# Kernel tuning notes

Measured on AMD Instinct MI355X. Metric: run time of the kernel, lower is better.

The kernel has to match this reference:

```python
import jax, jax.numpy as jnp
import numpy as np
from jax import lax

DN = ('NCHW', 'OIHW', 'NCHW')

def conv(x, w, groups=1):
    return lax.conv_general_dilated(x, w, (1, 1), 'SAME',
                                    feature_group_count=groups,
                                    dimension_numbers=DN)

def layernorm_cf(x, w, b, eps=1e-6):
    # channels-first LayerNorm over dim=1
    u = x.mean(1, keepdims=True)
    s = ((x - u) ** 2).mean(1, keepdims=True)
    xn = (x - u) / jnp.sqrt(s + eps)
    return w[None, :, None, None] * xn + b[None, :, None, None]

def l2norm(x, eps=1e-12):
    n = jnp.sqrt(jnp.sum(x * x, axis=-1, keepdims=True))
    return x / jnp.maximum(n, eps)

def setup_inputs() -> dict:
    key = jax.random.key(0)
    ks = jax.random.split(key, 16)
    B, C, H, W = 4, 192, 128, 128
    heads = 6
    hidden = int(C * 2.66)  # 510
    s = 0.02
    rn = lambda k, shp: jax.random.normal(k, shp, dtype=jnp.float32) * s
    return {
        'x': jax.random.normal(ks[0], (B, C, H, W), dtype=jnp.float32),
        'ln_w': jnp.ones((C,), jnp.float32),
        'ln_b': jnp.zeros((C,), jnp.float32),
        'temperature': jnp.ones((heads, 1, 1), jnp.float32),
        'q_w': rn(ks[1], (C, C, 1, 1)),
        'q_dw_w': rn(ks[2], (C, 1, 3, 3)),
        'kv_w': rn(ks[3], (2 * C, C, 1, 1)),
        'kv_dw_w': rn(ks[4], (2 * C, 1, 3, 3)),
        'proj_w': rn(ks[5], (C, C, 1, 1)),
        'pos_embed': rn(ks[6], (1, C, 1, 1)),
        'pos_q_w': rn(ks[7], (C, C, 1, 1)),
        'pos_k_w': rn(ks[8], (C, C, 1, 1)),
        'sel_in_w': rn(ks[9], (hidden, C, 3, 3)),
        'sel_dw_w': rn(ks[10], (hidden, 1, 3, 3)),
        'sel_out_w': rn(ks[11], (C, hidden, 3, 3)),
        'alpha': jnp.float32(0.5),
    }

def reference(x, ln_w, ln_b, temperature, q_w, q_dw_w, kv_w, kv_dw_w,
              proj_w, pos_embed, pos_q_w, pos_k_w,
              sel_in_w, sel_dw_w, sel_out_w, alpha):
    b, c, h, w = x.shape
    heads = temperature.shape[0]
    ch = c // heads
    n = h * w

    # --- CFA on norm_x (norm_x == norm_y since both are norm(x)) ---
    norm_x = layernorm_cf(x, ln_w, ln_b)
    q = conv(conv(norm_x, q_w), q_dw_w, groups=c)
    kv = conv(conv(norm_x, kv_w), kv_dw_w, groups=2 * c)
    k, v = jnp.split(kv, 2, axis=1)

    q = q.reshape(b, heads, ch, n)
    k = k.reshape(b, heads, ch, n)
    v = v.reshape(b, heads, ch, n)

    qn = l2norm(q)
    kn = l2norm(k)
    attn = jax.nn.softmax(jnp.einsum('bhcn,bhdn->bhcd', qn, kn) * temperature[None], axis=-1)
    out = jnp.einsum('bhcd,bhdn->bhcn', attn, v)

    pos_x = norm_x + pos_embed
    pos_q = conv(pos_x, pos_q_w).reshape(b, heads, ch, n)
    pos_k = conv(pos_x, pos_k_w).reshape(b, heads, ch, n)
    pos_attn = jax.nn.softmax(jnp.einsum('bhcn,bhdn->bhcd', pos_q, pos_k), axis=-1)
    pos_out = jnp.einsum('bhcd,bhdn->bhcn', pos_attn, v)

    out = (out + pos_out).reshape(b, c, h, w)
    out = conv(out, proj_w)
    x = x + alpha * out

    # --- SEL (conv-FFN) ---
    nx = layernorm_cf(x, ln_w, ln_b)
    g = conv(nx, sel_in_w)
    g = conv(g, sel_dw_w, groups=g.shape[1])
    g = jax.nn.silu(g)
    g = conv(g, sel_out_w)
    x = x + (1.0 - alpha) * g
    return x
```

## Files before the change

### kernel.cpp

```cpp
#include <hip/hip_runtime.h>
#include <hip/hip_bf16.h>
#include <stdint.h>

#define DEVI __device__ __forceinline__

typedef __attribute__((ext_vector_type(8))) unsigned short us8;
typedef __attribute__((ext_vector_type(8))) __bf16 bf16x8;
typedef __attribute__((ext_vector_type(4))) float f32x4;

#define BB 4
#define CC 192
#define HH 128
#define NPIX 16384
#define MTOT 65536
#define HEADS 6

DEVI float b2f(unsigned short u){ return __uint_as_float(((unsigned)u)<<16); }
DEVI unsigned short f2b(float f){
  unsigned u = __float_as_uint(f);
  return (unsigned short)((u + 0x7fffu + ((u>>16)&1u)) >> 16);
}

DEVI void gload16(const void* g, void* l){
  __builtin_amdgcn_global_load_lds((const __attribute__((address_space(1))) unsigned int*)g,
                                   (__attribute__((address_space(3))) unsigned int*)l,
                                   16, 0, 0);
}

__global__ __launch_bounds__(256)
void ln1_k(const float* __restrict__ x, const float* __restrict__ lnw,
           const float* __restrict__ lnb, unsigned short* __restrict__ nx)
{
  __shared__ float tile[CC*65];
  __shared__ float stats[64*2];
  int gbase = blockIdx.x * 64;
  int b = gbase >> 14; int n0 = gbase & (NPIX-1);
  for (int idx = threadIdx.x; idx < CC*64; idx += 256){
    int c = idx >> 6, j = idx & 63;
    tile[c*65 + j] = x[((size_t)b*CC + c)*NPIX + n0 + j];
  }
  __syncthreads();
  if (threadIdx.x < 64){
    int j = threadIdx.x;
    float s = 0.f, ss = 0.f;
    for (int c = 0; c < CC; c++){ float v = tile[c*65 + j]; s += v; ss += v*v; }
    float mu = s * (1.f/CC);
    float var = ss * (1.f/CC) - mu*mu;
    stats[j*2] = mu; stats[j*2+1] = rsqrtf(var + 1e-6f);
  }
  __syncthreads();
  for (int idx = threadIdx.x; idx < CC*64; idx += 256){
    int c = idx % CC, j = idx / CC;
    float v = (tile[c*65 + j] - stats[j*2]) * stats[j*2+1] * lnw[c] + lnb[c];
    nx[(size_t)(gbase + j)*CC + c] = f2b(v);
  }
}

__global__ __launch_bounds__(256)
void ln2_k(const float* __restrict__ x2, const float* __restrict__ lnw,
           const float* __restrict__ lnb, unsigned short* __restrict__ nx)
{
  int gm = blockIdx.x*4 + (threadIdx.x >> 6);
  int lane = threadIdx.x & 63;
  const float* row = x2 + (size_t)gm*CC;
  float v0 = row[lane], v1 = row[lane+64], v2 = row[lane+128];
  float s = v0+v1+v2, ss = v0*v0+v1*v1+v2*v2;
  #pragma unroll
  for (int o = 32; o >= 1; o >>= 1){
    s  += __shfl_xor(s,  o);
    ss += __shfl_xor(ss, o);
  }
  float mu = s * (1.f/CC);
  float rstd = rsqrtf(ss*(1.f/CC) - mu*mu + 1e-6f);
  unsigned short* o0 = nx + (size_t)gm*CC;
  o0[lane]     = f2b((v0-mu)*rstd*lnw[lane]     + lnb[lane]);
  o0[lane+64]  = f2b((v1-mu)*rstd*lnw[lane+64]  + lnb[lane+64]);
  o0[lane+128] = f2b((v2-mu)*rstd*lnw[lane+128] + lnb[lane+128]);
}

template<int EPI, int NSLICES>
__global__ __launch_bounds__(512, 2)
void gemm256_k(const unsigned short* __restrict__ A, int strideA,
               const unsigned short* __restrict__ W, int Ktot,
               int NcolsW, int NcolsStore, int outStride, int colBlocks,
               unsigned short* __restrict__ outB,
               const float* __restrict__ res, float* __restrict__ outF,
               const float* __restrict__ alphaP,
               const unsigned short* __restrict__ zerop)
{
  __shared__ unsigned short lds[65536];

  const int tid = threadIdx.x;
  const int l  = tid & 63;
  const int w  = tid >> 6;
  const int wm = w >> 2;
  const int wn = w & 3;

  const int q8 = gridDim.x >> 3;
  const int bid = (blockIdx.x & 7)*q8 + (blockIdx.x >> 3);
  const int mblk = bid / colBlocks;
  const int nblk = bid - mblk*colBlocks;
  const int m0 = mblk*256, co0 = nblk*256;

  int rowT[4], slotX[4];
  #pragma unroll
  for (int i = 0; i < 4; i++){
    rowT[i]  = (w*4 + i)*8 + (l >> 3);
    slotX[i] = (l & 7) ^ (rowT[i] & 7);
  }
  const unsigned short* baseA[4];
  int hhA[4], wwA[4];
  #pragma unroll
  for (int i = 0; i < 4; i++){
    int gm = m0 + rowT[i];
    int np = gm & (NPIX-1);
    hhA[i] = np >> 7; wwA[i] = np & 127;
    baseA[i] = A + (size_t)gm*strideA + (slotX[i] << 3);
  }
  const unsigned short* baseB[4];
  bool bval[4];
  #pragma unroll
  for (int i = 0; i < 4; i++){
    int co = co0 + rowT[i];
    bval[i] = (co < NcolsW);
    baseB[i] = bval[i] ? (W + (size_t)co*Ktot + (slotX[i] << 3)) : (zerop + (l << 3));
  }

  const int NT = Ktot >> 6;

  auto STAGE = [&](int ts){
    int buf = ts & 1;
    unsigned short* la = lds + buf*16384;
    unsigned short* lb = lds + 32768 + buf*16384;
    int ci0, dy = 0, dx = 0;
    if constexpr (NSLICES == 1){ ci0 = ts << 6; }
    else { int cib = ts/9, s = ts - cib*9; ci0 = cib << 6; dy = s/3 - 1; dx = s - (s/3)*3 - 1; }
    #pragma unroll
    for (int i = 0; i < 4; i++){
      const unsigned short* srcA;
      if constexpr (NSLICES == 1){
        srcA = baseA[i] + ci0;
      } else {
        int h2 = hhA[i] + dy, w2 = wwA[i] + dx;
        srcA = ((unsigned)h2 < 128u && (unsigned)w2 < 128u)
             ? (baseA[i] + (dy*HH + dx)*strideA + ci0)
             : (zerop + (l << 3));
      }
      gload16(srcA, la + (w*4 + i)*512);
    }
    #pragma unroll
    for (int i = 0; i < 4; i++){
      const unsigned short* srcB = bval[i] ? (baseB[i] + (ts << 6)) : baseB[i];
      gload16(srcB, lb + (w*4 + i)*512);
    }
  };

  f32x4 acc[8][4] = {};

  STAGE(0);
  asm volatile("s_waitcnt vmcnt(0)" ::: "memory");
  __syncthreads();

  for (int t = 0; t < NT; ++t){
    if (t + 1 < NT) STAGE(t + 1);
    const unsigned short* la = lds + (t & 1)*16384;
    const unsigned short* lb = lds + 32768 + (t & 1)*16384;
    __builtin_amdgcn_s_setprio(1);
    #pragma unroll
    for (int kk = 0; kk < 2; kk++){
      int ks = kk*4 + (l >> 4);
      bf16x8 bf[4];
      #pragma unroll
      for (int nf = 0; nf < 4; nf++){
        int rb = wn*64 + nf*16 + (l & 15);
        bf[nf] = *(const bf16x8*)(lb + rb*64 + ((ks ^ (rb & 7)) << 3));
      }
      #pragma unroll
      for (int mf = 0; mf < 8; mf++){
        int rm = wm*128 + mf*16 + (l & 15);
        bf16x8 af = *(const bf16x8*)(la + rm*64 + ((ks ^ (rm & 7)) << 3));
        #pragma unroll
        for (int nf = 0; nf < 4; nf++)
          acc[mf][nf] = __builtin_amdgcn_mfma_f32_16x16x32_bf16(af, bf[nf], acc[mf][nf], 0, 0, 0);
      }
    }
    __builtin_amdgcn_s_setprio(0);
    __syncthreads();
  }

  float alpha = (EPI == 2) ? (1.f - *alphaP) : 0.f;
  #pragma unroll
  for (int mf = 0; mf < 8; mf++){
    int r0 = m0 + wm*128 + mf*16 + ((l >> 4) << 2);
    #pragma unroll
    for (int nf = 0; nf < 4; nf++){
      int co = co0 + wn*64 + nf*16 + (l & 15);
      if (co < NcolsStore){
        #pragma unroll
        for (int r = 0; r < 4; r++){
          int gm = r0 + r;
          float v = acc[mf][nf][r];
          if constexpr (EPI == 0){
            outB[(size_t)gm*outStride + co] = f2b(v);
          } else {
            int b = gm >> 14, np = gm & (NPIX-1);
            outF[((size_t)b*CC + co)*NPIX + np] = res[(size_t)gm*CC + co] + alpha*v;
          }
        }
      }
    }
  }
}

template<int EPI, int NSLICES>
__global__ __launch_bounds__(256, 2)
void gemm_k(const unsigned short* __restrict__ A, int strideA,
            const unsigned short* __restrict__ W, int Ktot, int sliceC,
            int NcolsW, int NcolsStore, int outStride, int colBlocks,
            unsigned short* __restrict__ outB,
            const float* __restrict__ bias,
            const float* __restrict__ res,
            float* __restrict__ outF,
            const float* __restrict__ alphaP,
            const unsigned short* __restrict__ zerop)
{
  __shared__ unsigned short lds[2*128*64];
  unsigned short* ldsA = lds;
  unsigned short* ldsB = lds + 128*64;

  const int tid = threadIdx.x;
  const int lane = tid & 63;
  const int wv = tid >> 6;
  const int q8 = gridDim.x >> 3;
  const int bid = (blockIdx.x & 7)*q8 + (blockIdx.x >> 3);
  const int mblk = bid / colBlocks;
  const int nblk = bid - mblk*colBlocks;
  const int m0 = mblk*128, co0 = nblk*128;

  const int jT = lane & 7;
  int rowT[4];
  #pragma unroll
  for (int i = 0; i < 4; i++) rowT[i] = ((wv*4 + i)*64 + lane) >> 3;

  const unsigned short* bsrc[4];
  #pragma unroll
  for (int i = 0; i < 4; i++){
    int co = co0 + rowT[i];
    int jj = jT ^ (rowT[i] & 7);
    bsrc[i] = (co < NcolsW) ? (W + (size_t)co*Ktot + (jj << 3))
                            : (zerop + (lane << 3));
  }

  const unsigned short* asrc[4];
  int gmA[4], jjA[4];
  #pragma unroll
  for (int i = 0; i < 4; i++){
    gmA[i] = m0 + rowT[i];
    jjA[i] = jT ^ (rowT[i] & 7);
    asrc[i] = A + (size_t)gmA[i]*strideA + (jjA[i] << 3);
  }

  f32x4 acc[4][4] = {};
  int ci0 = 0, s = 0, dy = -1, dx = -1;

  for (int k0 = 0; k0 < Ktot; k0 += 64){
    if constexpr (NSLICES == 1){
      #pragma unroll
      for (int i = 0; i < 4; i++){
        gload16(asrc[i], (char*)ldsA + (wv*4 + i)*1024);
        asrc[i] += 64;
      }
    } else {
      #pragma unroll
      for (int i = 0; i < 4; i++){
        int gm = gmA[i];
        int np = gm & (NPIX-1);
        int hh = np >> 7, ww = np & 127;
        int h2 = hh + dy, w2 = ww + dx;
        const unsigned short* src = ((unsigned)h2 < 128u && (unsigned)w2 < 128u)
          ? (A + (size_t)(gm + dy*HH + dx)*strideA + ci0 + (jjA[i] << 3))
          : (zerop + (lane << 3));
        gload16(src, (char*)ldsA + (wv*4 + i)*1024);
      }
    }
    #pragma unroll
    for (int i = 0; i < 4; i++){
      gload16(bsrc[i], (char*)ldsB + (wv*4 + i)*1024);
      bsrc[i] += 64;
    }
    asm volatile("s_waitcnt vmcnt(0)" ::: "memory");
    __syncthreads();

    #pragma unroll
    for (int kk = 0; kk < 2; kk++){
      bf16x8 af[4], bfr[4];
      int kb = kk*64 + ((lane >> 4) << 4);
      #pragma unroll
      for (int mi = 0; mi < 4; mi++){
        int rm = (wv >> 1)*64 + mi*16 + (lane & 15);
        int off = rm*128 + (kb ^ ((rm & 7) << 4));
        af[mi] = *(const bf16x8*)((const char*)ldsA + off);
      }
      #pragma unroll
      for (int ni = 0; ni < 4; ni++){
        int rb = (wv & 1)*64 + ni*16 + (lane & 15);
        int off = rb*128 + (kb ^ ((rb & 7) << 4));
        bfr[ni] = *(const bf16x8*)((const char*)ldsB + off);
      }
      #pragma unroll
      for (int mi = 0; mi < 4; mi++)
        #pragma unroll
        for (int ni = 0; ni < 4; ni++)
          acc[mi][ni] = __builtin_amdgcn_mfma_f32_16x16x32_bf16(af[mi], bfr[ni], acc[mi][ni], 0, 0, 0);
    }
    __syncthreads();

    if constexpr (NSLICES > 1){
      s++; if (s == 9){ s = 0; ci0 += 64; }
      dy = s/3 - 1; dx = s - (s/3)*3 - 1;
    }
  }
  (void)sliceC;

  float alpha = 0.f;
  if (EPI == 1) alpha = *alphaP;
  if (EPI == 2) alpha = 1.f - *alphaP;
  const int colb = co0 + (wv & 1)*64;
  const int rowb = m0 + (wv >> 1)*64;
  #pragma unroll
  for (int mi = 0; mi < 4; mi++){
    int r0 = rowb + mi*16 + ((lane >> 4) << 2);
    #pragma unroll
    for (int ni = 0; ni < 4; ni++){
      int co = colb + ni*16 + (lane & 15);
      if (co < NcolsStore){
        float bv = (EPI == 0 && bias) ? bias[co] : 0.f;
        #pragma unroll
        for (int r = 0; r < 4; r++){
          int gm = r0 + r;
          float v = acc[mi][ni][r];
          if constexpr (EPI == 0){
            outB[(size_t)gm*outStride + co] = f2b(v + bv);
          } else if constexpr (EPI == 1){
            int b = gm >> 14, np = gm & (NPIX-1);
            outF[(size_t)gm*CC + co] = res[((size_t)b*CC + co)*NPIX + np] + alpha*v;
          } else {
            int b = gm >> 14, np = gm & (NPIX-1);
            outF[((size_t)b*CC + co)*NPIX + np] = res[(size_t)gm*CC + co] + alpha*v;
          }
        }
      }
    }
  }
}

template<int NCHV, int DOSILU>
__global__ __launch_bounds__(256)
void dw_k(const unsigned short* __restrict__ src, int strideS,
          const float* __restrict__ wtT, int wstride,
          unsigned short* __restrict__ dst, int strideD)
{
  const int q8 = gridDim.x >> 3;
  const int bid = (blockIdx.x & 7)*q8 + (blockIdx.x >> 3);
  int idx = bid*256 + threadIdx.x;
  int gm = idx / NCHV;
  int cb = idx - gm*NCHV;
  int c = cb*8;
  int np = gm & (NPIX-1);
  int hh = np >> 7, ww = np & 127;
  float acc[8] = {0,0,0,0,0,0,0,0};
  #pragma unroll
  for (int s = 0; s < 9; s++){
    int dy = s/3 - 1, dx = s%3 - 1;
    int h2 = hh + dy, w2 = ww + dx;
    if ((unsigned)h2 < 128u && (unsigned)w2 < 128u){
      us8 t = *(const us8*)(src + (size_t)(gm + dy*HH + dx)*strideS + c);
      f32x4 w0 = *(const f32x4*)(wtT + s*wstride + c);
      f32x4 w1 = *(const f32x4*)(wtT + s*wstride + c + 4);
      #pragma unroll
      for (int j = 0; j < 4; j++){
        acc[j]   += b2f(t[j])   * w0[j];
        acc[4+j] += b2f(t[4+j]) * w1[j];
      }
    }
  }
  us8 o;
  #pragma unroll
  for (int j = 0; j < 8; j++){
    float v = acc[j];
    if (DOSILU) v = v / (1.f + __expf(-v));
    o[j] = f2b(v);
  }
  *(us8*)(dst + (size_t)gm*strideD + c) = o;
}

__global__ __launch_bounds__(192)
void sumsq_k(const unsigned short* __restrict__ q, int stride, float* __restrict__ part)
{
  int b = blockIdx.x >> 5, ch = blockIdx.x & 31;
  int c = threadIdx.x;
  const unsigned short* base = q + ((size_t)b*NPIX + ch*512)*stride + c;
  float acc = 0.f;
  for (int r = 0; r < 512; r++){ float v = b2f(base[(size_t)r*stride]); acc += v*v; }
  part[(size_t)(b*32 + ch)*CC + c] = acc;
}

__global__ __launch_bounds__(256)
void pairdot_k(const unsigned short* __restrict__ qb, const unsigned short* __restrict__ kb,
               int stride, float* __restrict__ Spart)
{
  __shared__ float qs[32][129];
  __shared__ float ks[32][129];
  int bh = blockIdx.x >> 3;
  int chunk = blockIdx.x & 7;
  int b = bh / HEADS, h = bh - b*HEADS;
  int t = threadIdx.x;
  int cP = t >> 3;
  int dg = t & 7;
  size_t gm0 = (size_t)b*NPIX + chunk*2048;
  int r = t >> 1, hf = t & 1;
  float acc0=0, acc1=0, acc2=0, acc3=0;
  for (int sub = 0; sub < 16; sub++){
    __syncthreads();
    {
      const unsigned short* pq = qb + (gm0 + sub*128 + r)*stride + h*32 + hf*16;
      const unsigned short* pk = kb + (gm0 + sub*128 + r)*stride + h*32 + hf*16;
      us8 a0 = *(const us8*)pq; us8 a1 = *(const us8*)(pq + 8);
      us8 b0 = *(const us8*)pk; us8 b1 = *(const us8*)(pk + 8);
      #pragma unroll
      for (int j = 0; j < 8; j++){
        qs[hf*16 + j][r]     = b2f(a0[j]);
        qs[hf*16 + 8 + j][r] = b2f(a1[j]);
        ks[hf*16 + j][r]     = b2f(b0[j]);
        ks[hf*16 + 8 + j][r] = b2f(b1[j]);
      }
    }
    __syncthreads();
    for (int n = 0; n < 128; n++){
      float qv = qs[cP][n];
      acc0 += qv * ks[dg*4+0][n];
      acc1 += qv * ks[dg*4+1][n];
      acc2 += qv * ks[dg*4+2][n];
      acc3 += qv * ks[dg*4+3][n];
    }
  }
  float* o = Spart + (size_t)blockIdx.x*1024 + cP*32 + dg*4;
  o[0]=acc0; o[1]=acc1; o[2]=acc2; o[3]=acc3;
}

__global__ __launch_bounds__(64)
void smax_k(const float* __restrict__ Spos, const float* __restrict__ Scfa,
            const float* __restrict__ qnp, const float* __restrict__ knp,
            const float* __restrict__ temp, float* __restrict__ att)
{
  int bh = blockIdx.x; int b = bh / HEADS, h = bh - b*HEADS;
  __shared__ float kn[32];
  int t = threadIdx.x;
  if (t < 32){
    float ss = 0.f;
    for (int ck = 0; ck < 32; ck++) ss += knp[((size_t)b*32 + ck)*CC + h*32 + t];
    kn[t] = fmaxf(sqrtf(ss), 1e-12f);
  }
  __syncthreads();
  if (t >= 32) return;
  int c = t;
  float ssq = 0.f;
  for (int ck = 0; ck < 32; ck++) ssq += qnp[((size_t)b*32 + ck)*CC + h*32 + c];
  float qn = fmaxf(sqrtf(ssq), 1e-12f);
  float rowS[32], rowP[32];
  #pragma unroll
  for (int d = 0; d < 32; d++){
    float sv = 0.f, pv = 0.f;
    for (int ck = 0; ck < 8; ck++){
      sv += Scfa[(size_t)(bh*8 + ck)*1024 + c*32 + d];
      pv += Spos[(size_t)(bh*8 + ck)*1024 + c*32 + d];
    }
    rowS[d] = sv; rowP[d] = pv;
  }
  float tv = temp[h];
  float m1 = -3e38f, m2 = -3e38f;
  #pragma unroll
  for (int d = 0; d < 32; d++){
    rowS[d] = rowS[d] / (qn*kn[d]) * tv;
    m1 = fmaxf(m1, rowS[d]);
    m2 = fmaxf(m2, rowP[d]);
  }
  float s1 = 0.f, s2 = 0.f;
  #pragma unroll
  for (int d = 0; d < 32; d++){
    rowS[d] = __expf(rowS[d] - m1); s1 += rowS[d];
    rowP[d] = __expf(rowP[d] - m2); s2 += rowP[d];
  }
  float r1 = 1.f/s1, r2 = 1.f/s2;
  #pragma unroll
  for (int d = 0; d < 32; d++)
    att[(size_t)bh*1024 + c*32 + d] = rowS[d]*r1 + rowP[d]*r2;
}

__global__ __launch_bounds__(256)
void pv_k(const float* __restrict__ att, const unsigned short* __restrict__ vd, int stride,
          unsigned short* __restrict__ outT)
{
  __shared__ float As[32][33];
  int bh = blockIdx.x >> 8; int mc = blockIdx.x & 255;
  int b = bh / HEADS, h = bh - b*HEADS;
  int t = threadIdx.x;
  for (int i = t; i < 1024; i += 256) As[i >> 5][i & 31] = att[(size_t)bh*1024 + i];
  __syncthreads();
  int gm = b*NPIX + mc*64 + (t >> 2);
  int cq = t & 3;
  const unsigned short* vp = vd + (size_t)gm*stride + h*32;
  float acc[8] = {0,0,0,0,0,0,0,0};
  for (int d = 0; d < 32; d++){
    float vv = b2f(vp[d]);
    #pragma unroll
    for (int j = 0; j < 8; j++) acc[j] += As[cq*8 + j][d] * vv;
  }
  us8 o;
  #pragma unroll
  for (int j = 0; j < 8; j++) o[j] = f2b(acc[j]);
  *(us8*)(outT + (size_t)gm*CC + h*32 + cq*8) = o;
}

__global__ void castcopy_k(const float* __restrict__ s, unsigned short* __restrict__ d, int n){
  int i = blockIdx.x*256 + threadIdx.x; if (i < n) d[i] = f2b(s[i]);
}
__global__ void prepselin_k(const float* __restrict__ s, unsigned short* __restrict__ d){
  int i = blockIdx.x*256 + threadIdx.x;
  if (i >= 510*1728) return;
  int co = i / 1728, rem = i - co*1728;
  int chunk = rem >> 6, e = rem & 63;
  int cib = chunk / 9, sl = chunk - cib*9;
  int ci = cib*64 + e;
  d[i] = f2b(s[(size_t)(co*192 + ci)*9 + sl]);
}
__global__ void prepselout_k(const float* __restrict__ s, unsigned short* __restrict__ d){
  int i = blockIdx.x*256 + threadIdx.x;
  if (i >= 192*4608) return;
  int co = i / 4608, rem = i - co*4608;
  int chunk = rem >> 6, e = rem & 63;
  int cib = chunk / 9, sl = chunk - cib*9;
  int ci = cib*64 + e;
  d[i] = (ci < 510) ? f2b(s[(size_t)(co*510 + ci)*9 + sl]) : (unsigned short)0;
}
__global__ void prepbias_k(const float* __restrict__ pq, const float* __restrict__ pk,
                           const float* __restrict__ pe, float* __restrict__ bias){
  int r = blockIdx.x*64 + threadIdx.x;
  if (r >= 960) return;
  float s = 0.f;
  if (r < 384){
    const float* Wp = (r < 192) ? pq : pk;
    int co = (r < 192) ? r : r - 192;
    for (int ci = 0; ci < 192; ci++) s += Wp[co*192 + ci]*pe[ci];
  }
  bias[r] = s;
}
__global__ void prepdwT_k(const float* __restrict__ qdw, const float* __restrict__ kvdw,
                          const float* __restrict__ seldw,
                          float* __restrict__ wqkv, float* __restrict__ wsel){
  int i = blockIdx.x*256 + threadIdx.x;
  if (i < 9*576){
    int s = i / 576, c = i - s*576;
    wqkv[i] = (c < 192) ? qdw[c*9 + s] : kvdw[(size_t)(c-192)*9 + s];
  }
  int j = i - 9*576;
  if (j >= 0 && j < 9*512){
    int s = j / 512, c = j - s*512;
    wsel[j] = (c < 510) ? seldw[(size_t)c*9 + s] : 0.f;
  }
}

extern "C" void kernel_launch(void* const* d_in, const int* in_sizes, int n_in,
                              void* d_out, int out_size, void* d_ws, size_t ws_size,
                              hipStream_t stream)
{
  const float* x       = (const float*)d_in[0];
  const float* ln_w    = (const float*)d_in[1];
  const float* ln_b    = (const float*)d_in[2];
  const float* temp    = (const float*)d_in[3];
  const float* q_w     = (const float*)d_in[4];
  const float* q_dw    = (const float*)d_in[5];
  const float* kv_w    = (const float*)d_in[6];
  const float* kv_dw   = (const float*)d_in[7];
  const float* proj_w  = (const float*)d_in[8];
  const float* pos_e   = (const float*)d_in[9];
  const float* posq_w  = (const float*)d_in[10];
  const float* posk_w  = (const float*)d_in[11];
  const float* selin_w = (const float*)d_in[12];
  const float* seldw_w = (const float*)d_in[13];
  const float* selout_w= (const float*)d_in[14];
  const float* alphaP  = (const float*)d_in[15];

  char* ws = (char*)d_ws;
  unsigned short* zerop  = (unsigned short*)(ws + 0);
  float* biasC           = (float*)(ws + 4096);
  float* Spos            = (float*)(ws + 8192);
  float* Scfa            = (float*)(ws + 794624);
  float* qnp             = (float*)(ws + 1581056);
  float* knp             = (float*)(ws + 1679360);
  float* att             = (float*)(ws + 1777664);
  unsigned short* WC     = (unsigned short*)(ws + 2097152);
  unsigned short* Wproj  = (unsigned short*)(ws + 2465792);
  unsigned short* Wselin = (unsigned short*)(ws + 2539520);
  unsigned short* Wselout= (unsigned short*)(ws + 4302080);
  float* WdwQKV          = (float*)(ws + 6071552);
  float* WdwSEL          = (float*)(ws + 6092288);
  unsigned short* normx  = (unsigned short*)(ws + 8388608);
  unsigned short* outT   = normx;
  unsigned short* qp     = (unsigned short*)(ws + 33554432);
  float*          x2     = (float*)(ws + 33554432);
  unsigned short* nx     = (unsigned short*)(ws + 83886080);
  unsigned short* g2     = (unsigned short*)(ws + 83886080);
  unsigned short* qkvd   = (unsigned short*)(ws + 159383552);
  unsigned short* g      = qkvd;

  hipMemsetAsync(zerop, 0, 4096, stream);

  castcopy_k<<<144, 256, 0, stream>>>(posq_w, WC,          36864);
  castcopy_k<<<144, 256, 0, stream>>>(posk_w, WC + 36864,  36864);
  castcopy_k<<<144, 256, 0, stream>>>(q_w,    WC + 73728,  36864);
  castcopy_k<<<288, 256, 0, stream>>>(kv_w,   WC + 110592, 73728);
  castcopy_k<<<144, 256, 0, stream>>>(proj_w, Wproj,       36864);
  prepselin_k<<<3443, 256, 0, stream>>>(selin_w, Wselin);
  prepselout_k<<<3456, 256, 0, stream>>>(selout_w, Wselout);
  prepbias_k<<<15, 64, 0, stream>>>(posq_w, posk_w, pos_e, biasC);
  prepdwT_k<<<39, 256, 0, stream>>>(q_dw, kv_dw, seldw_w, WdwQKV, WdwSEL);

  ln1_k<<<1024, 256, 0, stream>>>(x, ln_w, ln_b, normx);
  gemm_k<0,1><<<512*8, 256, 0, stream>>>(normx, 192, WC, 192, 192, 960, 960, 960, 8,
                                         qp, biasC, nullptr, nullptr, nullptr, zerop);
  pairdot_k<<<192, 256, 0, stream>>>(qp, qp + 192, 960, Spos);
  dw_k<72,0><<<18432, 256, 0, stream>>>(qp + 384, 960, WdwQKV, 576, qkvd, 576);
  sumsq_k<<<128, 192, 0, stream>>>(qkvd,       576, qnp);
  sumsq_k<<<128, 192, 0, stream>>>(qkvd + 192, 576, knp);
  pairdot_k<<<192, 256, 0, stream>>>(qkvd, qkvd + 192, 576, Scfa);
  smax_k<<<24, 64, 0, stream>>>(Spos, Scfa, qnp, knp, temp, att);
  pv_k<<<24*256, 256, 0, stream>>>(att, qkvd + 384, 576, outT);
  gemm_k<1,1><<<512*2, 256, 0, stream>>>(outT, 192, Wproj, 192, 192, 192, 192, 0, 2,
                                         nullptr, nullptr, x, x2, alphaP, zerop);
  ln2_k<<<16384, 256, 0, stream>>>(x2, ln_w, ln_b, nx);
  gemm256_k<0,9><<<512, 512, 0, stream>>>(nx, 192, Wselin, 1728, 510, 512, 512, 2,
                                          g, nullptr, nullptr, alphaP, zerop);
  dw_k<64,1><<<16384, 256, 0, stream>>>(g, 512, WdwSEL, 512, g2, 512);
  gemm256_k<2,9><<<256, 512, 0, stream>>>(g2, 512, Wselout, 4608, 192, 192, 0, 1,
                                          nullptr, x2, (float*)d_out, alphaP, zerop);
}
```

Baseline: 878.5 us.

## Double-buffer small GEMM loads and rework pairdot into register-tiled reduction

The 128x128 gemm_k now double-buffers its A/B tiles in LDS, prefetching the next K step while computing the current one. It replaces the full vmcnt(0) waits and __syncthreads with partial vmcnt waits and raw barriers, and drops the unused multi-slice path. gemm256_k gets the same partial-wait barrier scheme. pairdot_k now keeps bf16 tiles in LDS and has each thread accumulate a 4x4 register tile over a quarter of the pixels, then reduces across waves. This replaces the per-element scalar loop over padded float arrays, cutting LDS traffic and conversion work at the cost of an extra cross-wave reduction step.

```diff
diff --git a/kernel.cpp b/kernel.cpp
--- a/kernel.cpp
+++ b/kernel.cpp
@@ -5,6 +5,7 @@
 #define DEVI __device__ __forceinline__
 
 typedef __attribute__((ext_vector_type(8))) unsigned short us8;
+typedef __attribute__((ext_vector_type(4))) unsigned short us4;
 typedef __attribute__((ext_vector_type(8))) __bf16 bf16x8;
 typedef __attribute__((ext_vector_type(4))) float f32x4;
 
@@ -158,11 +159,15 @@
   f32x4 acc[8][4] = {};
 
   STAGE(0);
-  asm volatile("s_waitcnt vmcnt(0)" ::: "memory");
-  __syncthreads();
-
   for (int t = 0; t < NT; ++t){
-    if (t + 1 < NT) STAGE(t + 1);
+    if (t + 1 < NT){
+      STAGE(t + 1);
+      asm volatile("s_waitcnt vmcnt(8)" ::: "memory");
+    } else {
+      asm volatile("s_waitcnt vmcnt(0)" ::: "memory");
+    }
+    __builtin_amdgcn_s_barrier();
+    asm volatile("" ::: "memory");
     const unsigned short* la = lds + (t & 1)*16384;
     const unsigned short* lb = lds + 32768 + (t & 1)*16384;
     __builtin_amdgcn_s_setprio(1);
@@ -185,7 +190,8 @@
       }
     }
     __builtin_amdgcn_s_setprio(0);
-    __syncthreads();
+    asm volatile("" ::: "memory");
+    __builtin_amdgcn_s_barrier();
   }
 
   float alpha = (EPI == 2) ? (1.f - *alphaP) : 0.f;
@@ -212,10 +218,10 @@
   }
 }
 
-template<int EPI, int NSLICES>
+template<int EPI>
 __global__ __launch_bounds__(256, 2)
 void gemm_k(const unsigned short* __restrict__ A, int strideA,
-            const unsigned short* __restrict__ W, int Ktot, int sliceC,
+            const unsigned short* __restrict__ W, int Ktot,
             int NcolsW, int NcolsStore, int outStride, int colBlocks,
             unsigned short* __restrict__ outB,
             const float* __restrict__ bias,
@@ -224,9 +230,7 @@
             const float* __restrict__ alphaP,
             const unsigned short* __restrict__ zerop)
 {
-  __shared__ unsigned short lds[2*128*64];
-  unsigned short* ldsA = lds;
-  unsigned short* ldsB = lds + 128*64;
+  __shared__ unsigned short lds[32768];
 
   const int tid = threadIdx.x;
   const int lane = tid & 63;
@@ -237,75 +241,60 @@
   const int nblk = bid - mblk*colBlocks;
   const int m0 = mblk*128, co0 = nblk*128;
 
-  const int jT = lane & 7;
-  int rowT[4];
-  #pragma unroll
-  for (int i = 0; i < 4; i++) rowT[i] = ((wv*4 + i)*64 + lane) >> 3;
-
-  const unsigned short* bsrc[4];
+  int rowT[4], slotX[4];
+  const unsigned short *baseA[4], *baseB[4];
+  bool bval[4];
   #pragma unroll
   for (int i = 0; i < 4; i++){
+    rowT[i]  = wv*32 + i*8 + (lane >> 3);
+    slotX[i] = (lane & 7) ^ (rowT[i] & 7);
+    baseA[i] = A + (size_t)(m0 + rowT[i])*strideA + (slotX[i] << 3);
     int co = co0 + rowT[i];
-    int jj = jT ^ (rowT[i] & 7);
-    bsrc[i] = (co < NcolsW) ? (W + (size_t)co*Ktot + (jj << 3))
-                            : (zerop + (lane << 3));
-  }
-
-  const unsigned short* asrc[4];
-  int gmA[4], jjA[4];
-  #pragma unroll
-  for (int i = 0; i < 4; i++){
-    gmA[i] = m0 + rowT[i];
-    jjA[i] = jT ^ (rowT[i] & 7);
-    asrc[i] = A + (size_t)gmA[i]*strideA + (jjA[i] << 3);
-  }
+    bval[i] = (co < NcolsW);
+    baseB[i] = bval[i] ? (W + (size_t)co*Ktot + (slotX[i] << 3)) : (zerop + (lane << 3));
+  }
+
+  const int NT = Ktot >> 6;
+
+  auto STAGE = [&](int ts){
+    unsigned short* la = lds + (ts & 1)*16384;
+    #pragma unroll
+    for (int i = 0; i < 4; i++)
+      gload16(baseA[i] + (ts << 6), (char*)la + (wv*4 + i)*1024);
+    #pragma unroll
+    for (int i = 0; i < 4; i++)
+      gload16(bval[i] ? (baseB[i] + (ts << 6)) : baseB[i],
+              (char*)la + 16384 + (wv*4 + i)*1024);
+  };
 
   f32x4 acc[4][4] = {};
-  int ci0 = 0, s = 0, dy = -1, dx = -1;
-
-  for (int k0 = 0; k0 < Ktot; k0 += 64){
-    if constexpr (NSLICES == 1){
-      #pragma unroll
-      for (int i = 0; i < 4; i++){
-        gload16(asrc[i], (char*)ldsA + (wv*4 + i)*1024);
-        asrc[i] += 64;
-      }
+
+  STAGE(0);
+  for (int t = 0; t < NT; ++t){
+    if (t + 1 < NT){
+      STAGE(t + 1);
+      asm volatile("s_waitcnt vmcnt(8)" ::: "memory");
     } else {
-      #pragma unroll
-      for (int i = 0; i < 4; i++){
-        int gm = gmA[i];
-        int np = gm & (NPIX-1);
-        int hh = np >> 7, ww = np & 127;
-        int h2 = hh + dy, w2 = ww + dx;
-        const unsigned short* src = ((unsigned)h2 < 128u && (unsigned)w2 < 128u)
-          ? (A + (size_t)(gm + dy*HH + dx)*strideA + ci0 + (jjA[i] << 3))
-          : (zerop + (lane << 3));
-        gload16(src, (char*)ldsA + (wv*4 + i)*1024);
-      }
-    }
-    #pragma unroll
-    for (int i = 0; i < 4; i++){
-      gload16(bsrc[i], (char*)ldsB + (wv*4 + i)*1024);
-      bsrc[i] += 64;
-    }
-    asm volatile("s_waitcnt vmcnt(0)" ::: "memory");
-    __syncthreads();
-
+      asm volatile("s_waitcnt vmcnt(0)" ::: "memory");
+    }
+    __builtin_amdgcn_s_barrier();
+    asm volatile("" ::: "memory");
+    const unsigned short* la = lds + (t & 1)*16384;
+    const unsigned short* lb = la + 8192;
+    __builtin_amdgcn_s_setprio(1);
     #pragma unroll
     for (int kk = 0; kk < 2; kk++){
+      int ks = kk*4 + (lane >> 4);
       bf16x8 af[4], bfr[4];
-      int kb = kk*64 + ((lane >> 4) << 4);
       #pragma unroll
       for (int mi = 0; mi < 4; mi++){
         int rm = (wv >> 1)*64 + mi*16 + (lane & 15);
-        int off = rm*128 + (kb ^ ((rm & 7) << 4));
-        af[mi] = *(const bf16x8*)((const char*)ldsA + off);
+        af[mi] = *(const bf16x8*)(la + rm*64 + ((ks ^ (rm & 7)) << 3));
       }
       #pragma unroll
       for (int ni = 0; ni < 4; ni++){
         int rb = (wv & 1)*64 + ni*16 + (lane & 15);
-        int off = rb*128 + (kb ^ ((rb & 7) << 4));
-        bfr[ni] = *(const bf16x8*)((const char*)ldsB + off);
+        bfr[ni] = *(const bf16x8*)(lb + rb*64 + ((ks ^ (rb & 7)) << 3));
       }
       #pragma unroll
       for (int mi = 0; mi < 4; mi++)
@@ -313,18 +302,13 @@
         for (int ni = 0; ni < 4; ni++)
           acc[mi][ni] = __builtin_amdgcn_mfma_f32_16x16x32_bf16(af[mi], bfr[ni], acc[mi][ni], 0, 0, 0);
     }
-    __syncthreads();
-
-    if constexpr (NSLICES > 1){
-      s++; if (s == 9){ s = 0; ci0 += 64; }
-      dy = s/3 - 1; dx = s - (s/3)*3 - 1;
-    }
-  }
-  (void)sliceC;
+    __builtin_amdgcn_s_setprio(0);
+    asm volatile("" ::: "memory");
+    __builtin_amdgcn_s_barrier();
+  }
 
   float alpha = 0.f;
   if (EPI == 1) alpha = *alphaP;
-  if (EPI == 2) alpha = 1.f - *alphaP;
   const int colb = co0 + (wv & 1)*64;
   const int rowb = m0 + (wv >> 1)*64;
   #pragma unroll
@@ -341,12 +325,9 @@
           float v = acc[mi][ni][r];
           if constexpr (EPI == 0){
             outB[(size_t)gm*outStride + co] = f2b(v + bv);
-          } else if constexpr (EPI == 1){
+          } else {
             int b = gm >> 14, np = gm & (NPIX-1);
             outF[(size_t)gm*CC + co] = res[((size_t)b*CC + co)*NPIX + np] + alpha*v;
-          } else {
-            int b = gm >> 14, np = gm & (NPIX-1);
-            outF[((size_t)b*CC + co)*NPIX + np] = res[(size_t)gm*CC + co] + alpha*v;
           }
         }
       }
@@ -409,43 +390,56 @@
 void pairdot_k(const unsigned short* __restrict__ qb, const unsigned short* __restrict__ kb,
                int stride, float* __restrict__ Spart)
 {
-  __shared__ float qs[32][129];
-  __shared__ float ks[32][129];
-  int bh = blockIdx.x >> 3;
-  int chunk = blockIdx.x & 7;
+  __shared__ unsigned short qt[4096];
+  __shared__ unsigned short kt[4096];
+  __shared__ float part[4][32][32];
+  int bh = blockIdx.x >> 3, chunk = blockIdx.x & 7;
   int b = bh / HEADS, h = bh - b*HEADS;
   int t = threadIdx.x;
-  int cP = t >> 3;
-  int dg = t & 7;
-  size_t gm0 = (size_t)b*NPIX + chunk*2048;
-  int r = t >> 1, hf = t & 1;
-  float acc0=0, acc1=0, acc2=0, acc3=0;
+  int w = t >> 6, l = t & 63;
+  int c4 = l >> 3, d4 = l & 7;
+  size_t gm0 = (size_t)b*NPIX + (size_t)chunk*2048;
+  int srow = t >> 2, scol = (t & 3) << 3;
+  float acc[4][4] = {};
   for (int sub = 0; sub < 16; sub++){
     __syncthreads();
-    {
-      const unsigned short* pq = qb + (gm0 + sub*128 + r)*stride + h*32 + hf*16;
-      const unsigned short* pk = kb + (gm0 + sub*128 + r)*stride + h*32 + hf*16;
-      us8 a0 = *(const us8*)pq; us8 a1 = *(const us8*)(pq + 8);
-      us8 b0 = *(const us8*)pk; us8 b1 = *(const us8*)(pk + 8);
-      #pragma unroll
-      for (int j = 0; j < 8; j++){
-        qs[hf*16 + j][r]     = b2f(a0[j]);
-        qs[hf*16 + 8 + j][r] = b2f(a1[j]);
-        ks[hf*16 + j][r]     = b2f(b0[j]);
-        ks[hf*16 + 8 + j][r] = b2f(b1[j]);
-      }
+    #pragma unroll
+    for (int hh2 = 0; hh2 < 2; hh2++){
+      size_t gr = gm0 + sub*128 + hh2*64 + srow;
+      us8 vq = *(const us8*)(qb + gr*stride + h*32 + scol);
+      us8 vk = *(const us8*)(kb + gr*stride + h*32 + scol);
+      *(us8*)(qt + hh2*2048 + t*8) = vq;
+      *(us8*)(kt + hh2*2048 + t*8) = vk;
     }
     __syncthreads();
-    for (int n = 0; n < 128; n++){
-      float qv = qs[cP][n];
-      acc0 += qv * ks[dg*4+0][n];
-      acc1 += qv * ks[dg*4+1][n];
-      acc2 += qv * ks[dg*4+2][n];
-      acc3 += qv * ks[dg*4+3][n];
-    }
-  }
-  float* o = Spart + (size_t)blockIdx.x*1024 + cP*32 + dg*4;
-  o[0]=acc0; o[1]=acc1; o[2]=acc2; o[3]=acc3;
+    #pragma unroll 4
+    for (int nn = 0; nn < 32; nn++){
+      int n = w*32 + nn;
+      us4 qv = *(const us4*)(qt + n*32 + c4*4);
+      us4 kv = *(const us4*)(kt + n*32 + d4*4);
+      float qf[4], kf[4];
+      #pragma unroll
+      for (int i = 0; i < 4; i++){ qf[i] = b2f(qv[i]); kf[i] = b2f(kv[i]); }
+      #pragma unroll
+      for (int i = 0; i < 4; i++)
+        #pragma unroll
+        for (int j = 0; j < 4; j++)
+          acc[i][j] += qf[i]*kf[j];
+    }
+  }
+  __syncthreads();
+  #pragma unroll
+  for (int i = 0; i < 4; i++)
+    #pragma unroll
+    for (int j = 0; j < 4; j++)
+      part[w][c4*4 + i][d4*4 + j] = acc[i][j];
+  __syncthreads();
+  #pragma unroll
+  for (int o = t; o < 1024; o += 256){
+    int c = o >> 5, d = o & 31;
+    Spart[(size_t)blockIdx.x*1024 + o] =
+      part[0][c][d] + part[1][c][d] + part[2][c][d] + part[3][c][d];
+  }
 }
 
 __global__ __launch_bounds__(64)
@@ -627,8 +621,8 @@
   prepdwT_k<<<39, 256, 0, stream>>>(q_dw, kv_dw, seldw_w, WdwQKV, WdwSEL);
 
   ln1_k<<<1024, 256, 0, stream>>>(x, ln_w, ln_b, normx);
-  gemm_k<0,1><<<512*8, 256, 0, stream>>>(normx, 192, WC, 192, 192, 960, 960, 960, 8,
-                                         qp, biasC, nullptr, nullptr, nullptr, zerop);
+  gemm_k<0><<<512*8, 256, 0, stream>>>(normx, 192, WC, 192, 960, 960, 960, 8,
+                                       qp, biasC, nullptr, nullptr, alphaP, zerop);
   pairdot_k<<<192, 256, 0, stream>>>(qp, qp + 192, 960, Spos);
   dw_k<72,0><<<18432, 256, 0, stream>>>(qp + 384, 960, WdwQKV, 576, qkvd, 576);
   sumsq_k<<<128, 192, 0, stream>>>(qkvd,       576, qnp);
@@ -636,8 +630,8 @@
   pairdot_k<<<192, 256, 0, stream>>>(qkvd, qkvd + 192, 576, Scfa);
   smax_k<<<24, 64, 0, stream>>>(Spos, Scfa, qnp, knp, temp, att);
   pv_k<<<24*256, 256, 0, stream>>>(att, qkvd + 384, 576, outT);
-  gemm_k<1,1><<<512*2, 256, 0, stream>>>(outT, 192, Wproj, 192, 192, 192, 192, 0, 2,
-                                         nullptr, nullptr, x, x2, alphaP, zerop);
+  gemm_k<1><<<512*2, 256, 0, stream>>>(outT, 192, Wproj, 192, 192, 192, 192, 2,
+                                       nullptr, nullptr, x, x2, alphaP, zerop);
   ln2_k<<<16384, 256, 0, stream>>>(x2, ln_w, ln_b, nx);
   gemm256_k<0,9><<<512, 512, 0, stream>>>(nx, 192, Wselin, 1728, 510, 512, 512, 2,
                                           g, nullptr, nullptr, alphaP, zerop);
```

Result: faster. 855.0 us (-2.7%).
